# Kernel optimization log

Measured on AMD Instinct MI355X. Metric: run time of the kernel, lower is better.

The kernel has to match this reference:

```python
import jax, jax.numpy as jnp
import numpy as np
import math

D_MODEL = 1024
H = 16
D_K = D_MODEL // H
SEQ = 4096
NEG = -1000000000.0  # mask constant from the original code


def setup_inputs() -> dict:
    key = jax.random.key(0)
    ks = jax.random.split(key, 7)
    return {
        "Q": jax.random.normal(ks[0], (SEQ, D_MODEL), dtype=jnp.float32),
        "K": jax.random.normal(ks[1], (SEQ, D_MODEL), dtype=jnp.float32),
        "V": jax.random.normal(ks[2], (SEQ, D_MODEL), dtype=jnp.float32),
        "W_Q": jax.random.normal(ks[3], (H, D_MODEL, D_K), dtype=jnp.float32),
        "W_K": jax.random.normal(ks[4], (H, D_MODEL, D_K), dtype=jnp.float32),
        "W_V": jax.random.normal(ks[5], (H, D_MODEL, D_K), dtype=jnp.float32),
        "W_O": jax.random.normal(ks[6], (D_MODEL, D_MODEL), dtype=jnp.float32),
        "mask": 1,
    }


def reference(Q, K, V, W_Q, W_K, W_V, W_O, mask):
    d_k = W_Q.shape[-1]
    s = Q.shape[0]
    # batched per-head projections: [h, s, d_k]
    Qh = jnp.einsum("sd,hdk->hsk", Q, W_Q)
    Kh = jnp.einsum("sd,hdk->hsk", K, W_K)
    Vh = jnp.einsum("sd,hdk->hsk", V, W_V)
    # scores: [h, s_q, s_k]
    scores = jnp.einsum("hqk,hsk->hqs", Qh, Kh) / math.sqrt(d_k)
    if mask:
        # faithful to torch: tril(scores) + triu(ones, 1) * -1e9
        lower = jnp.tril(jnp.ones((s, s), dtype=scores.dtype))
        upper = jnp.triu(jnp.ones((s, s), dtype=scores.dtype), k=1)
        scores = scores * lower + upper * NEG
    attn = jax.nn.softmax(scores, axis=-1)
    heads = jnp.einsum("hqs,hsk->hqk", attn, Vh)  # [h, s, d_k]
    # concat heads along feature dim in head order -> [s, h*d_k]
    concat = jnp.transpose(heads, (1, 0, 2)).reshape(s, -1)
    return concat @ W_O
```

## Files before the change

kernel.cpp:

```cpp
#include <hip/hip_runtime.h>
#include <hip/hip_bf16.h>

constexpr int S      = 4096;
constexpr int DMODEL = 1024;
constexpr int H      = 16;
constexpr int DK     = 64;

typedef __attribute__((ext_vector_type(8))) short          short8;
typedef __attribute__((ext_vector_type(4))) short          short4v;
typedef __attribute__((ext_vector_type(4))) float          float4v;
typedef __attribute__((ext_vector_type(4))) unsigned short ushort4v;
typedef __attribute__((ext_vector_type(8))) unsigned short ushort8;

__device__ __forceinline__ unsigned short f2bf(float x) {
    unsigned u = __builtin_bit_cast(unsigned, x);
    u += 0x7FFFu + ((u >> 16) & 1u);
    return (unsigned short)(u >> 16);
}
__device__ __forceinline__ float bf2f(unsigned short h) {
    unsigned u = ((unsigned)h) << 16;
    return __builtin_bit_cast(float, u);
}
__device__ __forceinline__ float fexp2(float x) { return __builtin_amdgcn_exp2f(x); }

__device__ __forceinline__ void gl_lds16(const unsigned short* g, unsigned short* l) {
    __builtin_amdgcn_global_load_lds(
        (const __attribute__((address_space(1))) unsigned int*)g,
        (__attribute__((address_space(3))) unsigned int*)l, 16, 0, 0);
}

__global__ __launch_bounds__(256) void prep_all(
    const float* __restrict__ Q, const float* __restrict__ K,
    const float* __restrict__ V,
    const float* __restrict__ WQ, const float* __restrict__ WK,
    const float* __restrict__ WV, const float* __restrict__ WO,
    unsigned short* __restrict__ QH, unsigned short* __restrict__ QL,
    unsigned short* __restrict__ KH, unsigned short* __restrict__ KL,
    unsigned short* __restrict__ Vb,
    unsigned short* __restrict__ WqtH, unsigned short* __restrict__ WqtL,
    unsigned short* __restrict__ WktH, unsigned short* __restrict__ WktL,
    unsigned short* __restrict__ Wvt,  unsigned short* __restrict__ WOt)
{
    const int zb = blockIdx.z;
    const int t  = threadIdx.x;

    if (zb < 3) {
        const size_t base = ((size_t)blockIdx.x * 256 + t) * 8;
        const float* src = (zb == 0) ? Q : (zb == 1) ? K : V;
        const float4 a = *(const float4*)(src + base);
        const float4 b = *(const float4*)(src + base + 4);
        const float xs[8] = {a.x, a.y, a.z, a.w, b.x, b.y, b.z, b.w};
        ushort8 hv, lv;
#pragma unroll
        for (int j = 0; j < 8; ++j) {
            const unsigned short h = f2bf(xs[j]);
            hv[j] = h;
            lv[j] = f2bf(xs[j] - bf2f(h));
        }
        if (zb == 0)      { *(ushort8*)(QH + base) = hv; *(ushort8*)(QL + base) = lv; }
        else if (zb == 1) { *(ushort8*)(KH + base) = hv; *(ushort8*)(KL + base) = lv; }
        else              { *(ushort8*)(Vb + base) = hv; }
        return;
    }

    const int bb = blockIdx.x;
    if (bb >= 1024) return;
    const int zfull = bb >> 4;
    const int which = zfull >> 4;
    const int z     = zfull & 15;
    const int r0    = (bb & 15) * 64;

    __shared__ float Ts[64][65];

    const float* in;
    unsigned short *oh, *ol;
    int z_mult, rstride;
    if (which == 0)      { in = WQ; oh = WqtH; ol = WqtL; z_mult = 65536; rstride = 64; }
    else if (which == 1) { in = WK; oh = WktH; ol = WktL; z_mult = 65536; rstride = 64; }
    else if (which == 2) { in = WV; oh = Wvt;  ol = nullptr; z_mult = 65536; rstride = 64; }
    else                 { in = WO; oh = WOt;  ol = nullptr; z_mult = 64;    rstride = 1024; }

    const float* src = in + (size_t)z * z_mult;
#pragma unroll
    for (int i = 0; i < 4; ++i) {
        const int row = (t >> 4) + i * 16;
        const int col = (t & 15) * 4;
        const float4 v = *(const float4*)&src[(size_t)(r0 + row) * rstride + col];
        Ts[row][col + 0] = v.x; Ts[row][col + 1] = v.y;
        Ts[row][col + 2] = v.z; Ts[row][col + 3] = v.w;
    }
    __syncthreads();
#pragma unroll
    for (int i = 0; i < 4; ++i) {
        const int c  = (t >> 4) + i * 16;
        const int rb = (t & 15) * 4;
        ushort4v hv, lv;
#pragma unroll
        for (int j = 0; j < 4; ++j) {
            const float x = Ts[rb + j][c];
            const unsigned short h = f2bf(x);
            hv[j] = h;
            lv[j] = f2bf(x - bf2f(h));
        }
        const size_t o = (size_t)(z * 64 + c) * 1024 + r0 + rb;
        *(ushort4v*)&oh[o] = hv;
        if (ol) *(ushort4v*)&ol[o] = lv;
    }
}

template <bool SPLIT, int EPI>
__device__ __forceinline__ void gemm_core(unsigned short* __restrict__ sm,
                                          const unsigned short* __restrict__ Ah,
                                          const unsigned short* __restrict__ Al,
                                          const unsigned short* __restrict__ Bh,
                                          const unsigned short* __restrict__ Bl,
                                          float* __restrict__ C,
                                          unsigned short* __restrict__ O1,
                                          unsigned short* __restrict__ O2,
                                          int m0, int n0)
{
    unsigned short* AsH = sm;
    unsigned short* BsH = sm + 4096;
    unsigned short* AsL = sm + 8192;
    unsigned short* BsL = sm + 12288;

    const int t    = threadIdx.x;
    const int wave = t >> 6;
    const int lane = t & 63;
    const int quad = lane >> 4;
    const int l15  = lane & 15;
    const int wm   = (wave & 1) * 64;
    const int wn   = (wave >> 1) * 64;

    float4v acc[4][4];
#pragma unroll
    for (int mi = 0; mi < 4; ++mi)
#pragma unroll
        for (int ni = 0; ni < 4; ++ni)
#pragma unroll
            for (int r = 0; r < 4; ++r) acc[mi][ni][r] = 0.f;

    for (int k0 = 0; k0 < 1024; k0 += 32) {
        __syncthreads();
#pragma unroll
        for (int i = 0; i < 2; ++i) {
            const int c   = t + 256 * i;
            const int row = c >> 2;
            const int kc  = (c & 3) * 8;
            const int lb  = (i * 256 + wave * 64) * 8;
            gl_lds16(&Ah[(size_t)(m0 + row) * 1024 + k0 + kc], AsH + lb);
            gl_lds16(&Bh[(size_t)(n0 + row) * 1024 + k0 + kc], BsH + lb);
            if (SPLIT) {
                gl_lds16(&Al[(size_t)(m0 + row) * 1024 + k0 + kc], AsL + lb);
                gl_lds16(&Bl[(size_t)(n0 + row) * 1024 + k0 + kc], BsL + lb);
            }
        }
        __syncthreads();

        short8 afh[4], bfh[4], afl[4], bfl[4];
#pragma unroll
        for (int mi = 0; mi < 4; ++mi)
            afh[mi] = *(const short8*)&AsH[(wm + mi * 16 + l15) * 32 + quad * 8];
#pragma unroll
        for (int ni = 0; ni < 4; ++ni)
            bfh[ni] = *(const short8*)&BsH[(wn + ni * 16 + l15) * 32 + quad * 8];
        if (SPLIT) {
#pragma unroll
            for (int mi = 0; mi < 4; ++mi)
                afl[mi] = *(const short8*)&AsL[(wm + mi * 16 + l15) * 32 + quad * 8];
#pragma unroll
            for (int ni = 0; ni < 4; ++ni)
                bfl[ni] = *(const short8*)&BsL[(wn + ni * 16 + l15) * 32 + quad * 8];
        }

#pragma unroll
        for (int mi = 0; mi < 4; ++mi)
#pragma unroll
            for (int ni = 0; ni < 4; ++ni) {
                acc[mi][ni] = __builtin_amdgcn_mfma_f32_16x16x32_bf16(
                    afh[mi], bfh[ni], acc[mi][ni], 0, 0, 0);
                if (SPLIT) {
                    acc[mi][ni] = __builtin_amdgcn_mfma_f32_16x16x32_bf16(
                        afh[mi], bfl[ni], acc[mi][ni], 0, 0, 0);
                    acc[mi][ni] = __builtin_amdgcn_mfma_f32_16x16x32_bf16(
                        afl[mi], bfh[ni], acc[mi][ni], 0, 0, 0);
                }
            }
    }

    if (EPI == 2) {
        __syncthreads();
        unsigned short* Ts = sm;
#pragma unroll
        for (int mi = 0; mi < 4; ++mi)
#pragma unroll
            for (int ni = 0; ni < 4; ++ni) {
                ushort4v pk;
#pragma unroll
                for (int r = 0; r < 4; ++r) pk[r] = f2bf(acc[mi][ni][r]);
                *(ushort4v*)&Ts[(wn + ni * 16 + l15) * 136 + wm + mi * 16 + quad * 4] = pk;
            }
        __syncthreads();
#pragma unroll
        for (int p = 0; p < 8; ++p) {
            const int n = p * 16 + (t >> 4);
            const int m = (t & 15) * 8;
            *(ushort8*)&O1[(size_t)(n0 + n) * 4096 + m0 + m] =
                *(const ushort8*)&Ts[n * 136 + m];
        }
        return;
    }

#pragma unroll
    for (int mi = 0; mi < 4; ++mi)
#pragma unroll
        for (int r = 0; r < 4; ++r) {
            const int m = m0 + wm + mi * 16 + quad * 4 + r;
            if (EPI == 0) {
                float* cp = C + (size_t)m * 1024 + n0 + wn + l15;
#pragma unroll
                for (int ni = 0; ni < 4; ++ni) cp[ni * 16] = acc[mi][ni][r];
            } else {
                unsigned short* o1 = O1 + (size_t)m * 1024 + n0 + wn + l15;
                unsigned short* o2 = O2 + (size_t)m * 1024 + n0 + wn + l15;
#pragma unroll
                for (int ni = 0; ni < 4; ++ni) {
                    const float v = acc[mi][ni][r];
                    const unsigned short hh = f2bf(v);
                    o1[ni * 16] = hh;
                    o2[ni * 16] = f2bf(v - bf2f(hh));
                }
            }
        }
}

__global__ __launch_bounds__(256) void proj_mfma(
    const unsigned short* __restrict__ XqH, const unsigned short* __restrict__ XqL,
    const unsigned short* __restrict__ XkH, const unsigned short* __restrict__ XkL,
    const unsigned short* __restrict__ Xv,
    const unsigned short* __restrict__ WqtH, const unsigned short* __restrict__ WqtL,
    const unsigned short* __restrict__ WktH, const unsigned short* __restrict__ WktL,
    const unsigned short* __restrict__ Wvt,
    float* __restrict__ Qc,
    unsigned short* __restrict__ KHg, unsigned short* __restrict__ KLg,
    unsigned short* __restrict__ Vt)
{
    __shared__ __align__(16) unsigned short smem[17408];
    const int m0 = blockIdx.x * 128, n0 = blockIdx.y * 128;
    if (blockIdx.z == 0)
        gemm_core<true, 0>(smem, XqH, XqL, WqtH, WqtL, Qc, nullptr, nullptr, m0, n0);
    else if (blockIdx.z == 1)
        gemm_core<true, 1>(smem, XkH, XkL, WktH, WktL, nullptr, KHg, KLg, m0, n0);
    else
        gemm_core<false, 2>(smem, Xv, nullptr, Wvt, nullptr, nullptr, Vt, nullptr, m0, n0);
}

__global__ __launch_bounds__(256) void out_gemm_mfma(
    const unsigned short* __restrict__ Ocb,
    const unsigned short* __restrict__ WOt,
    float* __restrict__ out)
{
    __shared__ __align__(16) unsigned short smem[2 * 4096];
    gemm_core<false, 0>(smem, Ocb, nullptr, WOt, nullptr, out, nullptr, nullptr,
                        blockIdx.x * 128, blockIdx.y * 128);
}

__global__ __launch_bounds__(256) void attn_mfma(const float* __restrict__ Qc,
                                                 const unsigned short* __restrict__ KHg,
                                                 const unsigned short* __restrict__ KLg,
                                                 const unsigned short* __restrict__ Vtg,
                                                 unsigned short* __restrict__ Ocb)
{
    __shared__ __align__(16) short Khi[64][72];
    __shared__ __align__(16) short Klo[64][72];
    __shared__ __align__(16) short Vts[64][72];
    __shared__ __align__(16) short Pb[4][16][72];

    const int bid = blockIdx.x;
    const int h   = bid & 15;
    const int qt  = 63 - (bid >> 4);
    const int q0  = qt * 64;

    const int t    = threadIdx.x;
    const int wave = t >> 6;
    const int lane = t & 63;
    const int quad = lane >> 4;
    const int l15  = lane & 15;

    constexpr float SCL = 0.18033688011112042f;

    short8 qhi[2], qlo[2];
    {
        const int qrow = q0 + wave * 16 + l15;
        const float* qp = Qc + (size_t)qrow * DMODEL + h * 64 + quad * 8;
#pragma unroll
        for (int ks = 0; ks < 2; ++ks) {
            float4 a = *(const float4*)(qp + ks * 32);
            float4 b = *(const float4*)(qp + ks * 32 + 4);
            const float xs[8] = {a.x, a.y, a.z, a.w, b.x, b.y, b.z, b.w};
#pragma unroll
            for (int j = 0; j < 8; ++j) {
                const unsigned short hi = f2bf(xs[j]);
                const unsigned short lo = f2bf(xs[j] - bf2f(hi));
                qhi[ks][j] = (short)hi;
                qlo[ks][j] = (short)lo;
            }
        }
    }

    short8 bones;
    {
        const short ob = (l15 == 0) ? (short)0x3F80 : (short)0;
#pragma unroll
        for (int j = 0; j < 8; ++j) bones[j] = ob;
    }

    float m_r[4] = {-1e30f, -1e30f, -1e30f, -1e30f};
    float4v lacc;
    float4v oacc[4];
#pragma unroll
    for (int r = 0; r < 4; ++r) lacc[r] = 0.f;
#pragma unroll
    for (int nt = 0; nt < 4; ++nt)
#pragma unroll
        for (int r = 0; r < 4; ++r) oacc[nt][r] = 0.f;

    const int srow = t >> 3;
    const int soff = (t & 7) * 8;

    ushort8 kh[2], kl[2], vt[2];
#pragma unroll
    for (int i = 0; i < 2; ++i) {
        const int row = srow + 32 * i;
        kh[i] = *(const ushort8*)&KHg[(size_t)row * 1024 + h * 64 + soff];
        kl[i] = *(const ushort8*)&KLg[(size_t)row * 1024 + h * 64 + soff];
        vt[i] = *(const ushort8*)&Vtg[(size_t)(h * 64 + row) * 4096 + soff];
    }

    for (int jt = 0; jt <= qt; ++jt) {
        const int j0 = jt * 64;
#pragma unroll
        for (int i = 0; i < 2; ++i) {
            const int row = srow + 32 * i;
            *(ushort8*)&Khi[row][soff] = kh[i];
            *(ushort8*)&Klo[row][soff] = kl[i];
            *(ushort8*)&Vts[row][soff] = vt[i];
        }
        __syncthreads();

        if (jt < qt) {
            const int jn = j0 + 64;
#pragma unroll
            for (int i = 0; i < 2; ++i) {
                const int row = srow + 32 * i;
                kh[i] = *(const ushort8*)&KHg[(size_t)(jn + row) * 1024 + h * 64 + soff];
                kl[i] = *(const ushort8*)&KLg[(size_t)(jn + row) * 1024 + h * 64 + soff];
                vt[i] = *(const ushort8*)&Vtg[(size_t)(h * 64 + row) * 4096 + jn + soff];
            }
        }

        float4v sacc[4];
#pragma unroll
        for (int nt = 0; nt < 4; ++nt)
#pragma unroll
            for (int r = 0; r < 4; ++r) sacc[nt][r] = 0.f;
        __builtin_amdgcn_s_setprio(1);
#pragma unroll
        for (int nt = 0; nt < 4; ++nt) {
            const int key = nt * 16 + l15;
#pragma unroll
            for (int ks = 0; ks < 2; ++ks) {
                const short8 bh = *(const short8*)&Khi[key][ks * 32 + quad * 8];
                const short8 bl = *(const short8*)&Klo[key][ks * 32 + quad * 8];
                sacc[nt] = __builtin_amdgcn_mfma_f32_16x16x32_bf16(qhi[ks], bh, sacc[nt], 0, 0, 0);
                sacc[nt] = __builtin_amdgcn_mfma_f32_16x16x32_bf16(qhi[ks], bl, sacc[nt], 0, 0, 0);
                sacc[nt] = __builtin_amdgcn_mfma_f32_16x16x32_bf16(qlo[ks], bh, sacc[nt], 0, 0, 0);
            }
        }
        __builtin_amdgcn_s_setprio(0);

        if (jt == qt) {
#pragma unroll
            for (int nt = 0; nt < 4; ++nt) {
                const int jg = j0 + nt * 16 + l15;
#pragma unroll
                for (int r = 0; r < 4; ++r) {
                    const int qg = q0 + wave * 16 + quad * 4 + r;
                    const float v = sacc[nt][r] * SCL;
                    sacc[nt][r] = (jg > qg) ? -1e9f : v;
                }
            }
        } else {
#pragma unroll
            for (int nt = 0; nt < 4; ++nt)
#pragma unroll
                for (int r = 0; r < 4; ++r)
                    sacc[nt][r] *= SCL;
        }

        float rmax[4];
#pragma unroll
        for (int r = 0; r < 4; ++r)
            rmax[r] = fmaxf(fmaxf(sacc[0][r], sacc[1][r]), fmaxf(sacc[2][r], sacc[3][r]));
#pragma unroll
        for (int off = 1; off < 16; off <<= 1)
#pragma unroll
            for (int r = 0; r < 4; ++r)
                rmax[r] = fmaxf(rmax[r], __shfl_xor(rmax[r], off));

        float alpha[4];
#pragma unroll
        for (int r = 0; r < 4; ++r) {
            const float mn = fmaxf(m_r[r], rmax[r]);
            alpha[r] = fexp2(m_r[r] - mn);
            m_r[r] = mn;
        }

#pragma unroll
        for (int nt = 0; nt < 4; ++nt)
#pragma unroll
            for (int r = 0; r < 4; ++r)
                sacc[nt][r] = fexp2(sacc[nt][r] - m_r[r]);

#pragma unroll
        for (int r = 0; r < 4; ++r) lacc[r] *= alpha[r];
#pragma unroll
        for (int nt = 0; nt < 4; ++nt)
#pragma unroll
            for (int r = 0; r < 4; ++r)
                oacc[nt][r] *= alpha[r];

#pragma unroll
        for (int nt = 0; nt < 4; ++nt)
#pragma unroll
            for (int r = 0; r < 4; ++r)
                Pb[wave][quad * 4 + r][nt * 16 + l15] = (short)f2bf(sacc[nt][r]);
        __asm__ volatile("s_waitcnt lgkmcnt(0)" ::: "memory");

        short8 af[2];
        af[0] = *(const short8*)&Pb[wave][l15][quad * 8];
        af[1] = *(const short8*)&Pb[wave][l15][32 + quad * 8];
        __builtin_amdgcn_s_setprio(1);
#pragma unroll
        for (int nt = 0; nt < 4; ++nt) {
            const int dk = nt * 16 + l15;
#pragma unroll
            for (int ks = 0; ks < 2; ++ks) {
                const short8 bv = *(const short8*)&Vts[dk][ks * 32 + quad * 8];
                oacc[nt] = __builtin_amdgcn_mfma_f32_16x16x32_bf16(af[ks], bv, oacc[nt], 0, 0, 0);
            }
        }
        lacc = __builtin_amdgcn_mfma_f32_16x16x32_bf16(af[0], bones, lacc, 0, 0, 0);
        lacc = __builtin_amdgcn_mfma_f32_16x16x32_bf16(af[1], bones, lacc, 0, 0, 0);
        __builtin_amdgcn_s_setprio(0);
        __syncthreads();
    }

#pragma unroll
    for (int r = 0; r < 4; ++r) {
        const float lsum = __shfl(lacc[r], (lane & 48));
        const float inv  = 1.0f / lsum;
        const int qg = q0 + wave * 16 + quad * 4 + r;
        unsigned short* op = Ocb + (size_t)qg * DMODEL + h * 64 + l15;
#pragma unroll
        for (int nt = 0; nt < 4; ++nt)
            op[nt * 16] = f2bf(oacc[nt][r] * inv);
    }
}

extern "C" void kernel_launch(void* const* d_in, const int* in_sizes, int n_in,
                              void* d_out, int out_size, void* d_ws, size_t ws_size,
                              hipStream_t stream)
{
    const float* Q  = (const float*)d_in[0];
    const float* K  = (const float*)d_in[1];
    const float* V  = (const float*)d_in[2];
    const float* WQ = (const float*)d_in[3];
    const float* WK = (const float*)d_in[4];
    const float* WV = (const float*)d_in[5];
    const float* WO = (const float*)d_in[6];

    float* out = (float*)d_out;

    const size_t SD4 = (size_t)S * DMODEL * 4;
    const size_t SD2 = (size_t)S * DMODEL * 2;
    const size_t W2  = (size_t)DMODEL * DMODEL * 2;
    char* p = (char*)d_ws;
    auto take = [&](size_t b) { char* r = p; p += b; return r; };

    float* Qc = (float*)take(SD4);
    unsigned short* KHg = (unsigned short*)take(SD2);
    unsigned short* KLg = (unsigned short*)take(SD2);
    unsigned short* Vtg = (unsigned short*)take(SD2);
    unsigned short* XqH = (unsigned short*)take(SD2);
    unsigned short* XqL = (unsigned short*)take(SD2);
    unsigned short* XkH = (unsigned short*)take(SD2);
    unsigned short* XkL = (unsigned short*)take(SD2);
    unsigned short* Xv  = (unsigned short*)take(SD2);
    unsigned short* WqtH = (unsigned short*)take(W2);
    unsigned short* WqtL = (unsigned short*)take(W2);
    unsigned short* WktH = (unsigned short*)take(W2);
    unsigned short* WktL = (unsigned short*)take(W2);
    unsigned short* Wvt  = (unsigned short*)take(W2);
    unsigned short* WOt  = (unsigned short*)take(W2);
    unsigned short* Ocb  = (unsigned short*)take(SD2);

    prep_all<<<dim3(2048, 1, 4), 256, 0, stream>>>(
        Q, K, V, WQ, WK, WV, WO,
        XqH, XqL, XkH, XkL, Xv, WqtH, WqtL, WktH, WktL, Wvt, WOt);
    proj_mfma<<<dim3(S / 128, DMODEL / 128, 3), 256, 0, stream>>>(
        XqH, XqL, XkH, XkL, Xv, WqtH, WqtL, WktH, WktL, Wvt, Qc, KHg, KLg, Vtg);
    attn_mfma<<<dim3((S / 64) * H), 256, 0, stream>>>(Qc, KHg, KLg, Vtg, Ocb);
    out_gemm_mfma<<<dim3(S / 128, DMODEL / 128), 256, 0, stream>>>(Ocb, WOt, out);
}
```

Baseline: 335.6 us.

## Use 128-query attention tiles with 8 waves sharing each K/V tile

Attention blocks now cover 128 query rows with 512 threads (8 waves), so each staged K/V tile in shared memory serves twice as many queries. This halves the global K/V traffic per query. The block order also interleaves long and short causal rows to balance the work. Waves whose queries all lie above the diagonal still iterate over the extra key tile and get fully masked, so the diagonal region does some wasted work. The setprio hints are removed as well.

```diff
diff --git a/kernel.cpp b/kernel.cpp
--- a/kernel.cpp
+++ b/kernel.cpp
@@ -265,7 +265,7 @@
                         blockIdx.x * 128, blockIdx.y * 128);
 }
 
-__global__ __launch_bounds__(256) void attn_mfma(const float* __restrict__ Qc,
+__global__ __launch_bounds__(512) void attn_mfma(const float* __restrict__ Qc,
                                                  const unsigned short* __restrict__ KHg,
                                                  const unsigned short* __restrict__ KLg,
                                                  const unsigned short* __restrict__ Vtg,
@@ -274,12 +274,14 @@
     __shared__ __align__(16) short Khi[64][72];
     __shared__ __align__(16) short Klo[64][72];
     __shared__ __align__(16) short Vts[64][72];
-    __shared__ __align__(16) short Pb[4][16][72];
+    __shared__ __align__(16) short Pb[8][16][72];
 
     const int bid = blockIdx.x;
     const int h   = bid & 15;
-    const int qt  = 63 - (bid >> 4);
-    const int q0  = qt * 64;
+    const int g   = bid >> 4;
+    const int qb  = (g < 16) ? (31 - g) : (g - 16);
+    const int q0  = qb * 128;
+    const int jtmax = 2 * qb + 1;
 
     const int t    = threadIdx.x;
     const int wave = t >> 6;
@@ -328,35 +330,23 @@
     const int srow = t >> 3;
     const int soff = (t & 7) * 8;
 
-    ushort8 kh[2], kl[2], vt[2];
-#pragma unroll
-    for (int i = 0; i < 2; ++i) {
-        const int row = srow + 32 * i;
-        kh[i] = *(const ushort8*)&KHg[(size_t)row * 1024 + h * 64 + soff];
-        kl[i] = *(const ushort8*)&KLg[(size_t)row * 1024 + h * 64 + soff];
-        vt[i] = *(const ushort8*)&Vtg[(size_t)(h * 64 + row) * 4096 + soff];
-    }
-
-    for (int jt = 0; jt <= qt; ++jt) {
+    ushort8 kh, kl, vt;
+    kh = *(const ushort8*)&KHg[(size_t)srow * 1024 + h * 64 + soff];
+    kl = *(const ushort8*)&KLg[(size_t)srow * 1024 + h * 64 + soff];
+    vt = *(const ushort8*)&Vtg[(size_t)(h * 64 + srow) * 4096 + soff];
+
+    for (int jt = 0; jt <= jtmax; ++jt) {
         const int j0 = jt * 64;
-#pragma unroll
-        for (int i = 0; i < 2; ++i) {
-            const int row = srow + 32 * i;
-            *(ushort8*)&Khi[row][soff] = kh[i];
-            *(ushort8*)&Klo[row][soff] = kl[i];
-            *(ushort8*)&Vts[row][soff] = vt[i];
-        }
+        *(ushort8*)&Khi[srow][soff] = kh;
+        *(ushort8*)&Klo[srow][soff] = kl;
+        *(ushort8*)&Vts[srow][soff] = vt;
         __syncthreads();
 
-        if (jt < qt) {
+        if (jt < jtmax) {
             const int jn = j0 + 64;
-#pragma unroll
-            for (int i = 0; i < 2; ++i) {
-                const int row = srow + 32 * i;
-                kh[i] = *(const ushort8*)&KHg[(size_t)(jn + row) * 1024 + h * 64 + soff];
-                kl[i] = *(const ushort8*)&KLg[(size_t)(jn + row) * 1024 + h * 64 + soff];
-                vt[i] = *(const ushort8*)&Vtg[(size_t)(h * 64 + row) * 4096 + jn + soff];
-            }
+            kh = *(const ushort8*)&KHg[(size_t)(jn + srow) * 1024 + h * 64 + soff];
+            kl = *(const ushort8*)&KLg[(size_t)(jn + srow) * 1024 + h * 64 + soff];
+            vt = *(const ushort8*)&Vtg[(size_t)(h * 64 + srow) * 4096 + jn + soff];
         }
 
         float4v sacc[4];
@@ -364,7 +354,6 @@
         for (int nt = 0; nt < 4; ++nt)
 #pragma unroll
             for (int r = 0; r < 4; ++r) sacc[nt][r] = 0.f;
-        __builtin_amdgcn_s_setprio(1);
 #pragma unroll
         for (int nt = 0; nt < 4; ++nt) {
             const int key = nt * 16 + l15;
@@ -377,9 +366,8 @@
                 sacc[nt] = __builtin_amdgcn_mfma_f32_16x16x32_bf16(qlo[ks], bh, sacc[nt], 0, 0, 0);
             }
         }
-        __builtin_amdgcn_s_setprio(0);
-
-        if (jt == qt) {
+
+        if (j0 + 63 > q0 + wave * 16) {
 #pragma unroll
             for (int nt = 0; nt < 4; ++nt) {
                 const int jg = j0 + nt * 16 + l15;
@@ -440,7 +428,6 @@
         short8 af[2];
         af[0] = *(const short8*)&Pb[wave][l15][quad * 8];
         af[1] = *(const short8*)&Pb[wave][l15][32 + quad * 8];
-        __builtin_amdgcn_s_setprio(1);
 #pragma unroll
         for (int nt = 0; nt < 4; ++nt) {
             const int dk = nt * 16 + l15;
@@ -452,7 +439,6 @@
         }
         lacc = __builtin_amdgcn_mfma_f32_16x16x32_bf16(af[0], bones, lacc, 0, 0, 0);
         lacc = __builtin_amdgcn_mfma_f32_16x16x32_bf16(af[1], bones, lacc, 0, 0, 0);
-        __builtin_amdgcn_s_setprio(0);
         __syncthreads();
     }
 
@@ -510,6 +496,6 @@
         XqH, XqL, XkH, XkL, Xv, WqtH, WqtL, WktH, WktL, Wvt, WOt);
     proj_mfma<<<dim3(S / 128, DMODEL / 128, 3), 256, 0, stream>>>(
         XqH, XqL, XkH, XkL, Xv, WqtH, WqtL, WktH, WktL, Wvt, Qc, KHg, KLg, Vtg);
-    attn_mfma<<<dim3((S / 64) * H), 256, 0, stream>>>(Qc, KHg, KLg, Vtg, Ocb);
+    attn_mfma<<<dim3((S / 128) * H), 512, 0, stream>>>(Qc, KHg, KLg, Vtg, Ocb);
     out_gemm_mfma<<<dim3(S / 128, DMODEL / 128), 256, 0, stream>>>(Ocb, WOt, out);
 }
```

New measurement: 332.9 us. About the same (-0.8%).
